# Kernel optimization log

Measured on AMD Instinct MI355X. Metric: run time of the kernel, lower is better.

## Reference

```python
import jax, jax.numpy as jnp
import numpy as np

B, S, D, F, E, K = 4, 2048, 768, 3072, 8, 2
LB_W, Z_W = 0.01, 0.001


def setup_inputs() -> dict:
    key = jax.random.key(0)
    ks = jax.random.split(key, 6)
    x = jax.random.normal(ks[0], (B, S, D), dtype=jnp.float32)
    Wr = jax.random.truncated_normal(ks[1], -2.0, 2.0, (D, E), dtype=jnp.float32) * 0.02
    W1 = jax.random.normal(ks[2], (E, D, F), dtype=jnp.float32) * (1.0 / np.sqrt(D))
    b1 = jnp.zeros((E, F), dtype=jnp.float32)
    W2 = jax.random.normal(ks[3], (E, F, D), dtype=jnp.float32) * (1.0 / np.sqrt(F))
    b2 = jnp.zeros((E, D), dtype=jnp.float32)
    return {"x": x, "Wr": Wr, "W1": W1, "b1": b1, "W2": W2, "b2": b2}


def reference(x, Wr, W1, b1, W2, b2):
    # Router
    router_logits = jnp.einsum('bsd,de->bse', x, Wr)            # [B,S,E]
    router_probs = jax.nn.softmax(router_logits, axis=-1)
    top_k_probs, top_k_idx = jax.lax.top_k(router_probs, K)     # [B,S,K]
    top_k_probs = top_k_probs / (jnp.sum(top_k_probs, axis=-1, keepdims=True) + 1e-8)

    # Auxiliary losses
    expert_usage = jnp.mean(router_probs, axis=(0, 1))          # [E]
    mean_usage = jnp.mean(expert_usage)
    var_usage = jnp.mean(jnp.square(expert_usage - mean_usage))
    lb_loss = var_usage / (mean_usage * mean_usage + 1e-8) * jnp.float32(E)
    z_loss = jnp.mean(jnp.square(jax.nn.logsumexp(router_logits, axis=-1)))

    # Combine weights per expert: sum over top-k slots assigned to expert e
    one_hot = jax.nn.one_hot(top_k_idx, E, dtype=x.dtype)       # [B,S,K,E]
    combine = jnp.sum(one_hot * top_k_probs[..., None], axis=2) # [B,S,E]

    # Expert FFNs (loop over fixed small E, vectorized over tokens)
    output = jnp.zeros_like(x)
    for e in range(E):
        h = jax.nn.gelu(jnp.einsum('bsd,df->bsf', x, W1[e]) + b1[e], approximate=False)
        y = jnp.einsum('bsf,fd->bsd', h, W2[e]) + b2[e]
        output = output + y * combine[..., e:e + 1]

    aux = {"load_balancing_loss": lb_loss * LB_W, "router_z_loss": z_loss * Z_W}
    return output, aux["load_balancing_loss"], aux["router_z_loss"]
```

## Files before the change

### kernel.cpp

```cpp
#include <hip/hip_runtime.h>
#include <cstdint>
#include <cstddef>

#define B_ 4
#define S_ 2048
#define D_ 768
#define F_ 3072
#define E_ 8
#define NTOK (B_*S_)
#define NASSIGN (NTOK*2)
#define RBLK 256
#define FBLK 32
#define MAXTILE 136

typedef unsigned short u16;
typedef __attribute__((ext_vector_type(8))) __bf16 bf16x8;
typedef __attribute__((ext_vector_type(4))) float f32x4;

__device__ __forceinline__ u16 f2bf(float f) {
    unsigned int u = __builtin_bit_cast(unsigned int, f);
    u += 0x7fffu + ((u >> 16) & 1u);
    return (u16)(u >> 16);
}

__device__ __forceinline__ void async16(const void* g, void* l) {
    __builtin_amdgcn_global_load_lds(
        (const __attribute__((address_space(1))) unsigned int*)g,
        (__attribute__((address_space(3))) unsigned int*)l, 16, 0, 0);
}

__device__ __forceinline__ float gelu_f(float v) {
    float z = v * 0.70710678f;
    float a = fabsf(z);
    float t = __builtin_amdgcn_rcpf(1.0f + 0.3275911f * a);
    float poly = t * (0.254829592f + t * (-0.284496736f + t * (1.421413741f +
                 t * (-1.453152027f + t * 1.061405429f))));
    float e = __expf(-z * z);
    float erf_z = copysignf(1.0f - poly * e, z);
    return 0.5f * v * (1.0f + erf_z);
}

__global__ void k_init(int* cursors) {
    int t = threadIdx.x;
    if (t < E_) cursors[t] = 0;
}

__global__ void k_cvt_x(const float* __restrict__ x, u16* __restrict__ xb) {
    int id = blockIdx.x * 256 + threadIdx.x;
    float4 v = ((const float4*)x)[id];
    ushort4 o;
    o.x = f2bf(v.x); o.y = f2bf(v.y); o.z = f2bf(v.z); o.w = f2bf(v.w);
    ((ushort4*)xb)[id] = o;
}

__global__ void k_tcvt(const float* __restrict__ in, u16* __restrict__ out, int R, int C) {
    __shared__ u16 t[32][33];
    int e = blockIdx.z;
    int c0 = blockIdx.x * 32, r0 = blockIdx.y * 32;
    int tx = threadIdx.x & 7;
    int ty = threadIdx.x >> 3;
    const float* ip = in + (size_t)e * R * C + (size_t)(r0 + ty) * C + c0 + tx * 4;
    float4 v = *(const float4*)ip;
    t[tx * 4 + 0][ty] = f2bf(v.x);
    t[tx * 4 + 1][ty] = f2bf(v.y);
    t[tx * 4 + 2][ty] = f2bf(v.z);
    t[tx * 4 + 3][ty] = f2bf(v.w);
    __syncthreads();
    u16* op = out + (size_t)e * C * R + (size_t)(c0 + ty) * R + r0 + tx * 4;
    ushort4 o;
    o.x = t[ty][tx * 4 + 0]; o.y = t[ty][tx * 4 + 1];
    o.z = t[ty][tx * 4 + 2]; o.w = t[ty][tx * 4 + 3];
    *(ushort4*)op = o;
}

__global__ __launch_bounds__(256) void k_router(
    const float* __restrict__ x, const float* __restrict__ Wr,
    float* __restrict__ usage_part,
    float* __restrict__ z_part,
    int*   __restrict__ hist_part,
    int* __restrict__ tk_idx, float* __restrict__ tk_w)
{
    __shared__ float wrt[E_ * D_];
    __shared__ float s_usage[E_];
    __shared__ float s_z;
    __shared__ int   s_hist[E_];
    int tid = threadIdx.x;
    for (int i = tid; i < E_ * D_; i += 256) {
        int d = i >> 3, e = i & 7;
        wrt[e * D_ + d] = Wr[i];
    }
    if (tid < E_) { s_usage[tid] = 0.f; s_hist[tid] = 0; }
    if (tid == 0) s_z = 0.f;
    __syncthreads();

    int w = tid >> 6, lane = tid & 63;
    float u_acc[E_];
    #pragma unroll
    for (int e = 0; e < E_; e++) u_acc[e] = 0.f;
    float z_acc = 0.f;

    for (int it = 0; it < 8; it++) {
        int tok = blockIdx.x * 32 + it * 4 + w;
        float acc[E_];
        #pragma unroll
        for (int e = 0; e < E_; e++) acc[e] = 0.f;
        const float* xr = x + (size_t)tok * D_;
        for (int d = lane; d < D_; d += 64) {
            float xv = xr[d];
            #pragma unroll
            for (int e = 0; e < E_; e++) acc[e] += xv * wrt[e * D_ + d];
        }
        #pragma unroll
        for (int off = 32; off > 0; off >>= 1) {
            #pragma unroll
            for (int e = 0; e < E_; e++) acc[e] += __shfl_down(acc[e], off);
        }
        if (lane == 0) {
            float m = acc[0];
            #pragma unroll
            for (int e = 1; e < E_; e++) m = fmaxf(m, acc[e]);
            float p[E_], s = 0.f;
            #pragma unroll
            for (int e = 0; e < E_; e++) { p[e] = expf(acc[e] - m); s += p[e]; }
            float inv = 1.f / s;
            #pragma unroll
            for (int e = 0; e < E_; e++) { p[e] *= inv; u_acc[e] += p[e]; }
            float lse = m + logf(s);
            z_acc += lse * lse;
            int i1 = 0;
            for (int e = 1; e < E_; e++) if (p[e] > p[i1]) i1 = e;
            int i2 = -1;
            for (int e = 0; e < E_; e++) {
                if (e == i1) continue;
                if (i2 < 0 || p[e] > p[i2]) i2 = e;
            }
            float denom = p[i1] + p[i2] + 1e-8f;
            tk_idx[tok * 2 + 0] = i1; tk_idx[tok * 2 + 1] = i2;
            tk_w[tok * 2 + 0] = p[i1] / denom;
            tk_w[tok * 2 + 1] = p[i2] / denom;
            atomicAdd(&s_hist[i1], 1); atomicAdd(&s_hist[i2], 1);
        }
    }
    if (lane == 0) {
        #pragma unroll
        for (int e = 0; e < E_; e++) atomicAdd(&s_usage[e], u_acc[e]);
        atomicAdd(&s_z, z_acc);
    }
    __syncthreads();
    if (tid < E_) {
        usage_part[blockIdx.x * E_ + tid] = s_usage[tid];
        hist_part[blockIdx.x * E_ + tid]  = s_hist[tid];
    }
    if (tid == 0) z_part[blockIdx.x] = s_z;
}

__global__ __launch_bounds__(256) void k_finalize(
    const float* __restrict__ usage_part, const float* __restrict__ z_part,
    const int* __restrict__ hist_part,
    int* __restrict__ counts, int* __restrict__ offsets,
    int* __restrict__ tile_list,
    float* __restrict__ out_scalars)
{
    __shared__ float s_u[E_];
    __shared__ float s_z;
    __shared__ int   s_h[E_];
    int tid = threadIdx.x;
    if (tid < E_) { s_u[tid] = 0.f; s_h[tid] = 0; }
    if (tid == 0) s_z = 0.f;
    __syncthreads();

    float u[E_]; int h[E_];
    #pragma unroll
    for (int e = 0; e < E_; e++) { u[e] = usage_part[tid * E_ + e]; h[e] = hist_part[tid * E_ + e]; }
    float z = z_part[tid];
    #pragma unroll
    for (int off = 32; off > 0; off >>= 1) {
        #pragma unroll
        for (int e = 0; e < E_; e++) {
            u[e] += __shfl_down(u[e], off);
            h[e] += __shfl_down(h[e], off);
        }
        z += __shfl_down(z, off);
    }
    if ((tid & 63) == 0) {
        #pragma unroll
        for (int e = 0; e < E_; e++) { atomicAdd(&s_u[e], u[e]); atomicAdd(&s_h[e], h[e]); }
        atomicAdd(&s_z, z);
    }
    __syncthreads();
    if (tid == 0) {
        int o = 0, nt = 0;
        for (int e = 0; e < E_; e++) {
            int c = s_h[e];
            counts[e] = c; offsets[e] = o; o += c;
            for (int m0 = 0; m0 < c; m0 += 128) tile_list[1 + nt++] = (m0 << 8) | e;
        }
        tile_list[0] = nt;
        float uu[E_], mean = 0.f;
        for (int e = 0; e < E_; e++) { uu[e] = s_u[e] / (float)NTOK; mean += uu[e]; }
        mean /= (float)E_;
        float var = 0.f;
        for (int e = 0; e < E_; e++) { float d = uu[e] - mean; var += d * d; }
        var /= (float)E_;
        out_scalars[0] = var / (mean * mean + 1e-8f) * (float)E_ * 0.01f;
        out_scalars[1] = (s_z / (float)NTOK) * 0.001f;
    }
}

__global__ __launch_bounds__(256) void k_fill(
    const int* __restrict__ tk_idx, const float* __restrict__ tk_w,
    const int* __restrict__ offsets, int* __restrict__ cursors,
    int* __restrict__ assign_token, float* __restrict__ assign_weight,
    int* __restrict__ pos)
{
    __shared__ int l_cnt[E_];
    __shared__ int l_base[E_];
    int tid = threadIdx.x;
    if (tid < E_) l_cnt[tid] = 0;
    __syncthreads();
    int t = blockIdx.x * 256 + tid;
    int e0 = tk_idx[t * 2 + 0], e1 = tk_idx[t * 2 + 1];
    int r0 = atomicAdd(&l_cnt[e0], 1);
    int r1 = atomicAdd(&l_cnt[e1], 1);
    __syncthreads();
    if (tid < E_) l_base[tid] = atomicAdd(&cursors[tid], l_cnt[tid]);
    __syncthreads();
    int row0 = offsets[e0] + l_base[e0] + r0;
    int row1 = offsets[e1] + l_base[e1] + r1;
    assign_token[row0] = t; assign_weight[row0] = tk_w[t * 2 + 0]; pos[t * 2 + 0] = row0;
    assign_token[row1] = t; assign_weight[row1] = tk_w[t * 2 + 1]; pos[t * 2 + 1] = row1;
}

__global__ __launch_bounds__(256) void k_gemm1(
    const u16* __restrict__ xb, const u16* __restrict__ w1t,
    const float* __restrict__ b1,
    const int* __restrict__ counts, const int* __restrict__ offsets,
    const int* __restrict__ tile_list,
    const int* __restrict__ assign_token, u16* __restrict__ h)
{
    int nt = tile_list[0];
    if ((int)blockIdx.x >= nt) return;
    int packed = tile_list[1 + blockIdx.x];
    int e = packed & 0xff;
    int m0 = packed >> 8;
    int cnt = counts[e];
    int off = offsets[e];
    int n0 = blockIdx.y * 128;

    __shared__ __align__(16) u16 As[2][128 * 32];
    __shared__ __align__(16) u16 Bs[2][128 * 32];

    int tid = threadIdx.x;
    int w = tid >> 6, lane = tid & 63;
    int rA = lane >> 2;
    int colk = (lane & 3) * 8;
    int r0 = (w * 2 + 0) * 16 + rA;
    int r1 = (w * 2 + 1) * 16 + rA;

    int c0b = __builtin_amdgcn_readfirstlane((w * 2 + 0) * 1024);
    int c1b = __builtin_amdgcn_readfirstlane((w * 2 + 1) * 1024);

    int g0 = m0 + r0; if (g0 > cnt - 1) g0 = cnt - 1;
    int g1 = m0 + r1; if (g1 > cnt - 1) g1 = cnt - 1;
    const u16* agp0 = xb + (size_t)assign_token[off + g0] * D_ + colk;
    const u16* agp1 = xb + (size_t)assign_token[off + g1] * D_ + colk;
    const u16* bgp0 = w1t + ((size_t)e * F_ + n0 + r0) * D_ + colk;
    const u16* bgp1 = w1t + ((size_t)e * F_ + n0 + r1) * D_ + colk;

    f32x4 acc[4][4];
    #pragma unroll
    for (int i = 0; i < 4; i++)
        #pragma unroll
        for (int j = 0; j < 4; j++) acc[i][j] = (f32x4){0.f, 0.f, 0.f, 0.f};

    int wm = (w >> 1) * 64, wn = (w & 1) * 64;
    int fm = lane & 15, k8 = (lane >> 4) * 8;

    #define STAGE1(buf, kk) do { \
        async16(agp0 + (kk), (char*)As[buf] + c0b); \
        async16(agp1 + (kk), (char*)As[buf] + c1b); \
        async16(bgp0 + (kk), (char*)Bs[buf] + c0b); \
        async16(bgp1 + (kk), (char*)Bs[buf] + c1b); \
    } while (0)
    #define COMPUTE1(buf) do { \
        bf16x8 af[4], bfr[4]; \
        _Pragma("unroll") \
        for (int i = 0; i < 4; i++) af[i] = *(const bf16x8*)&As[buf][(wm + i * 16 + fm) * 32 + k8]; \
        _Pragma("unroll") \
        for (int j = 0; j < 4; j++) bfr[j] = *(const bf16x8*)&Bs[buf][(wn + j * 16 + fm) * 32 + k8]; \
        _Pragma("unroll") \
        for (int i = 0; i < 4; i++) \
            _Pragma("unroll") \
            for (int j = 0; j < 4; j++) \
                acc[i][j] = __builtin_amdgcn_mfma_f32_16x16x32_bf16(af[i], bfr[j], acc[i][j], 0, 0, 0); \
    } while (0)

    STAGE1(0, 0);
    __syncthreads();
    for (int kk = 0; kk < D_; kk += 64) {
        STAGE1(1, kk + 32);
        COMPUTE1(0);
        __syncthreads();
        if (kk + 64 < D_) STAGE1(0, kk + 64);
        COMPUTE1(1);
        __syncthreads();
    }
    #undef STAGE1
    #undef COMPUTE1

    int rbase = (lane >> 4) * 4;
    #pragma unroll
    for (int j = 0; j < 4; j++) {
        int f = n0 + wn + j * 16 + fm;
        float bias = b1[e * F_ + f];
        #pragma unroll
        for (int i = 0; i < 4; i++) {
            #pragma unroll
            for (int r = 0; r < 4; r++) {
                int m = m0 + wm + i * 16 + rbase + r;
                if (m < cnt) {
                    float v = acc[i][j][r] + bias;
                    h[(size_t)(off + m) * F_ + f] = f2bf(gelu_f(v));
                }
            }
        }
    }
}

__global__ __launch_bounds__(256) void k_gemm2(
    const u16* __restrict__ h, const u16* __restrict__ w2t,
    const float* __restrict__ b2,
    const int* __restrict__ counts, const int* __restrict__ offsets,
    const int* __restrict__ tile_list,
    const float* __restrict__ assign_weight, float* __restrict__ y)
{
    int nt = tile_list[0];
    if ((int)blockIdx.x >= nt) return;
    int packed = tile_list[1 + blockIdx.x];
    int e = packed & 0xff;
    int m0 = packed >> 8;
    int cnt = counts[e];
    int off = offsets[e];
    int n0 = blockIdx.y * 128;

    __shared__ __align__(16) u16 As[2][128 * 32];
    __shared__ __align__(16) u16 Bs[2][128 * 32];

    int tid = threadIdx.x;
    int w = tid >> 6, lane = tid & 63;
    int rA = lane >> 2;
    int colk = (lane & 3) * 8;
    int r0 = (w * 2 + 0) * 16 + rA;
    int r1 = (w * 2 + 1) * 16 + rA;

    int c0b = __builtin_amdgcn_readfirstlane((w * 2 + 0) * 1024);
    int c1b = __builtin_amdgcn_readfirstlane((w * 2 + 1) * 1024);

    const u16* agp0 = h + (size_t)(off + m0 + r0) * F_ + colk;
    const u16* agp1 = h + (size_t)(off + m0 + r1) * F_ + colk;
    const u16* bgp0 = w2t + ((size_t)e * D_ + n0 + r0) * F_ + colk;
    const u16* bgp1 = w2t + ((size_t)e * D_ + n0 + r1) * F_ + colk;

    f32x4 acc[4][4];
    #pragma unroll
    for (int i = 0; i < 4; i++)
        #pragma unroll
        for (int j = 0; j < 4; j++) acc[i][j] = (f32x4){0.f, 0.f, 0.f, 0.f};

    int wm = (w >> 1) * 64, wn = (w & 1) * 64;
    int fm = lane & 15, k8 = (lane >> 4) * 8;

    #define STAGE2(buf, kk) do { \
        async16(agp0 + (kk), (char*)As[buf] + c0b); \
        async16(agp1 + (kk), (char*)As[buf] + c1b); \
        async16(bgp0 + (kk), (char*)Bs[buf] + c0b); \
        async16(bgp1 + (kk), (char*)Bs[buf] + c1b); \
    } while (0)
    #define COMPUTE2(buf) do { \
        bf16x8 af[4], bfr[4]; \
        _Pragma("unroll") \
        for (int i = 0; i < 4; i++) af[i] = *(const bf16x8*)&As[buf][(wm + i * 16 + fm) * 32 + k8]; \
        _Pragma("unroll") \
        for (int j = 0; j < 4; j++) bfr[j] = *(const bf16x8*)&Bs[buf][(wn + j * 16 + fm) * 32 + k8]; \
        _Pragma("unroll") \
        for (int i = 0; i < 4; i++) \
            _Pragma("unroll") \
            for (int j = 0; j < 4; j++) \
                acc[i][j] = __builtin_amdgcn_mfma_f32_16x16x32_bf16(af[i], bfr[j], acc[i][j], 0, 0, 0); \
    } while (0)

    STAGE2(0, 0);
    __syncthreads();
    for (int kk = 0; kk < F_; kk += 64) {
        STAGE2(1, kk + 32);
        COMPUTE2(0);
        __syncthreads();
        if (kk + 64 < F_) STAGE2(0, kk + 64);
        COMPUTE2(1);
        __syncthreads();
    }
    #undef STAGE2
    #undef COMPUTE2

    int rbase = (lane >> 4) * 4;
    #pragma unroll
    for (int j = 0; j < 4; j++) {
        int d = n0 + wn + j * 16 + fm;
        float bias = b2[e * D_ + d];
        #pragma unroll
        for (int i = 0; i < 4; i++) {
            #pragma unroll
            for (int r = 0; r < 4; r++) {
                int m = m0 + wm + i * 16 + rbase + r;
                if (m < cnt) {
                    float wgt = assign_weight[off + m];
                    y[(size_t)(off + m) * D_ + d] = (acc[i][j][r] + bias) * wgt;
                }
            }
        }
    }
}

__global__ void k_combine(const float* __restrict__ y, const int* __restrict__ pos,
                          float* __restrict__ out)
{
    int g = blockIdx.x * 256 + threadIdx.x;
    int t = g / 192, c = g - t * 192;
    int p0 = pos[t * 2], p1 = pos[t * 2 + 1];
    const float4* y4 = (const float4*)y;
    float4 a = y4[(size_t)p0 * 192 + c];
    float4 b = y4[(size_t)p1 * 192 + c];
    float4 o = {a.x + b.x, a.y + b.y, a.z + b.z, a.w + b.w};
    ((float4*)out)[g] = o;
}

extern "C" void kernel_launch(void* const* d_in, const int* in_sizes, int n_in,
                              void* d_out, int out_size, void* d_ws, size_t ws_size,
                              hipStream_t stream)
{
    const float* x  = (const float*)d_in[0];
    const float* Wr = (const float*)d_in[1];
    const float* W1 = (const float*)d_in[2];
    const float* b1 = (const float*)d_in[3];
    const float* W2 = (const float*)d_in[4];
    const float* b2 = (const float*)d_in[5];
    float* out = (float*)d_out;

    char* base = (char*)d_ws;
    size_t o = 0;
    auto alloc = [&](size_t bytes) {
        char* r = base + o;
        o += (bytes + 255) & ~(size_t)255;
        return r;
    };
    int*   counts        = (int*)  alloc(E_ * 4);
    int*   cursors       = (int*)  alloc(E_ * 4);
    int*   offsets       = (int*)  alloc(E_ * 4);
    int*   tile_list     = (int*)  alloc(256 * 4);
    float* usage_part    = (float*)alloc((size_t)RBLK * E_ * 4);
    float* z_part        = (float*)alloc((size_t)RBLK * 4);
    int*   hist_part     = (int*)  alloc((size_t)RBLK * E_ * 4);
    int*   tk_idx        = (int*)  alloc((size_t)NTOK * 2 * 4);
    float* tk_w          = (float*)alloc((size_t)NTOK * 2 * 4);
    int*   pos           = (int*)  alloc((size_t)NTOK * 2 * 4);
    int*   assign_token  = (int*)  alloc((size_t)NASSIGN * 4);
    float* assign_weight = (float*)alloc((size_t)NASSIGN * 4);
    u16*   xb            = (u16*)  alloc((size_t)NTOK * D_ * 2);
    u16*   w1t           = (u16*)  alloc((size_t)E_ * F_ * D_ * 2);
    u16*   w2t           = (u16*)  alloc((size_t)E_ * D_ * F_ * 2);
    u16*   hbuf          = (u16*)  alloc((size_t)NASSIGN * F_ * 2);
    float* y             = (float*)alloc((size_t)NASSIGN * D_ * 4);

    k_init<<<dim3(1), dim3(64), 0, stream>>>(cursors);
    k_cvt_x<<<dim3(NTOK * D_ / 1024), dim3(256), 0, stream>>>(x, xb);
    k_tcvt<<<dim3(F_ / 32, D_ / 32, E_), dim3(256), 0, stream>>>(W1, w1t, D_, F_);
    k_tcvt<<<dim3(D_ / 32, F_ / 32, E_), dim3(256), 0, stream>>>(W2, w2t, F_, D_);
    k_router<<<dim3(RBLK), dim3(256), 0, stream>>>(x, Wr, usage_part, z_part, hist_part, tk_idx, tk_w);
    k_finalize<<<dim3(1), dim3(256), 0, stream>>>(usage_part, z_part, hist_part, counts, offsets,
                                                  tile_list, out + (size_t)NTOK * D_);
    k_fill<<<dim3(FBLK), dim3(256), 0, stream>>>(tk_idx, tk_w, offsets, cursors, assign_token, assign_weight, pos);
    k_gemm1<<<dim3(MAXTILE, F_ / 128), dim3(256), 0, stream>>>(xb, w1t, b1, counts, offsets, tile_list,
                                                               assign_token, hbuf);
    k_gemm2<<<dim3(MAXTILE, D_ / 128), dim3(256), 0, stream>>>(hbuf, w2t, b2, counts, offsets, tile_list,
                                                               assign_weight, y);
    k_combine<<<dim3(NTOK * D_ / 1024), dim3(256), 0, stream>>>(y, pos, out);
}
```

Before: 624.0 us.

## Swizzle LDS tiles, stage gemm1 epilogue via LDS, fuse combine into gemm2 atomics

Applies an XOR swizzle to the LDS tile layout in both grouped GEMMs to cut bank conflicts on the MFMA fragment reads. The gemm1 epilogue is staged through LDS so GELU outputs go to global memory as 16-byte row stores instead of scattered 2-byte writes. The gemm2 epilogue scatters weighted results straight into the output with float atomic adds after a memset, which removes the y buffer, the pos array and the combine kernel. The atomics add contention and make the float summation order nondeterministic, and hbuf is padded to cover the tail tile's writes.

Result: faster. 611.6 us (-2.0%).

```diff
diff --git a/kernel.cpp b/kernel.cpp
--- a/kernel.cpp
+++ b/kernel.cpp
@@ -75,9 +75,8 @@
 
 __global__ __launch_bounds__(256) void k_router(
     const float* __restrict__ x, const float* __restrict__ Wr,
-    float* __restrict__ usage_part,
-    float* __restrict__ z_part,
-    int*   __restrict__ hist_part,
+    float* __restrict__ usage_part, float* __restrict__ z_part,
+    int* __restrict__ hist_part,
     int* __restrict__ tk_idx, float* __restrict__ tk_w)
 {
     __shared__ float wrt[E_ * D_];
@@ -210,8 +209,7 @@
 __global__ __launch_bounds__(256) void k_fill(
     const int* __restrict__ tk_idx, const float* __restrict__ tk_w,
     const int* __restrict__ offsets, int* __restrict__ cursors,
-    int* __restrict__ assign_token, float* __restrict__ assign_weight,
-    int* __restrict__ pos)
+    int* __restrict__ assign_token, float* __restrict__ assign_weight)
 {
     __shared__ int l_cnt[E_];
     __shared__ int l_base[E_];
@@ -227,8 +225,8 @@
     __syncthreads();
     int row0 = offsets[e0] + l_base[e0] + r0;
     int row1 = offsets[e1] + l_base[e1] + r1;
-    assign_token[row0] = t; assign_weight[row0] = tk_w[t * 2 + 0]; pos[t * 2 + 0] = row0;
-    assign_token[row1] = t; assign_weight[row1] = tk_w[t * 2 + 1]; pos[t * 2 + 1] = row1;
+    assign_token[row0] = t; assign_weight[row0] = tk_w[t * 2 + 0];
+    assign_token[row1] = t; assign_weight[row1] = tk_w[t * 2 + 1];
 }
 
 __global__ __launch_bounds__(256) void k_gemm1(
@@ -247,13 +245,13 @@
     int off = offsets[e];
     int n0 = blockIdx.y * 128;
 
-    __shared__ __align__(16) u16 As[2][128 * 32];
-    __shared__ __align__(16) u16 Bs[2][128 * 32];
+    __shared__ __align__(16) u16 SM[16384];
+    char* smb = (char*)SM;
 
     int tid = threadIdx.x;
     int w = tid >> 6, lane = tid & 63;
     int rA = lane >> 2;
-    int colk = (lane & 3) * 8;
+    int colk = ((lane & 3) ^ (rA & 3)) * 8;
     int r0 = (w * 2 + 0) * 16 + rA;
     int r1 = (w * 2 + 1) * 16 + rA;
 
@@ -274,20 +272,23 @@
         for (int j = 0; j < 4; j++) acc[i][j] = (f32x4){0.f, 0.f, 0.f, 0.f};
 
     int wm = (w >> 1) * 64, wn = (w & 1) * 64;
-    int fm = lane & 15, k8 = (lane >> 4) * 8;
+    int fm = lane & 15;
+    int slot = ((lane >> 4) ^ (fm & 3)) * 8;
 
     #define STAGE1(buf, kk) do { \
-        async16(agp0 + (kk), (char*)As[buf] + c0b); \
-        async16(agp1 + (kk), (char*)As[buf] + c1b); \
-        async16(bgp0 + (kk), (char*)Bs[buf] + c0b); \
-        async16(bgp1 + (kk), (char*)Bs[buf] + c1b); \
+        async16(agp0 + (kk), smb + (buf) * 8192 + c0b); \
+        async16(agp1 + (kk), smb + (buf) * 8192 + c1b); \
+        async16(bgp0 + (kk), smb + 16384 + (buf) * 8192 + c0b); \
+        async16(bgp1 + (kk), smb + 16384 + (buf) * 8192 + c1b); \
     } while (0)
     #define COMPUTE1(buf) do { \
+        const u16* Ab = SM + (buf) * 4096; \
+        const u16* Bb = SM + 8192 + (buf) * 4096; \
         bf16x8 af[4], bfr[4]; \
         _Pragma("unroll") \
-        for (int i = 0; i < 4; i++) af[i] = *(const bf16x8*)&As[buf][(wm + i * 16 + fm) * 32 + k8]; \
-        _Pragma("unroll") \
-        for (int j = 0; j < 4; j++) bfr[j] = *(const bf16x8*)&Bs[buf][(wn + j * 16 + fm) * 32 + k8]; \
+        for (int i = 0; i < 4; i++) af[i] = *(const bf16x8*)&Ab[(wm + i * 16 + fm) * 32 + slot]; \
+        _Pragma("unroll") \
+        for (int j = 0; j < 4; j++) bfr[j] = *(const bf16x8*)&Bb[(wn + j * 16 + fm) * 32 + slot]; \
         _Pragma("unroll") \
         for (int i = 0; i < 4; i++) \
             _Pragma("unroll") \
@@ -309,21 +310,30 @@
     #undef COMPUTE1
 
     int rbase = (lane >> 4) * 4;
-    #pragma unroll
-    for (int j = 0; j < 4; j++) {
-        int f = n0 + wn + j * 16 + fm;
-        float bias = b1[e * F_ + f];
-        #pragma unroll
-        for (int i = 0; i < 4; i++) {
+    u16* tb = SM + w * 4096;
+    float biasv[4];
+    #pragma unroll
+    for (int j = 0; j < 4; j++) biasv[j] = b1[e * F_ + n0 + wn + j * 16 + fm];
+    #pragma unroll
+    for (int i = 0; i < 4; i++)
+        #pragma unroll
+        for (int j = 0; j < 4; j++)
             #pragma unroll
             for (int r = 0; r < 4; r++) {
-                int m = m0 + wm + i * 16 + rbase + r;
-                if (m < cnt) {
-                    float v = acc[i][j][r] + bias;
-                    h[(size_t)(off + m) * F_ + f] = f2bf(gelu_f(v));
-                }
+                int m_l = i * 16 + rbase + r;
+                int f_l = j * 16 + fm;
+                u16 q = f2bf(gelu_f(acc[i][j][r] + biasv[j]));
+                tb[m_l * 64 + ((((f_l >> 3) ^ (m_l & 7)) << 3) | (f_l & 7))] = q;
             }
-        }
+    __syncthreads();
+    #pragma unroll
+    for (int s = 0; s < 8; s++) {
+        int m_l = s * 8 + (lane >> 3);
+        int c = lane & 7;
+        uint4 vv = *(const uint4*)&tb[m_l * 64 + ((c ^ (m_l & 7)) << 3)];
+        int m = m0 + wm + m_l;
+        if (m < cnt)
+            *(uint4*)&h[(size_t)(off + m) * F_ + n0 + wn + c * 8] = vv;
     }
 }
 
@@ -332,7 +342,8 @@
     const float* __restrict__ b2,
     const int* __restrict__ counts, const int* __restrict__ offsets,
     const int* __restrict__ tile_list,
-    const float* __restrict__ assign_weight, float* __restrict__ y)
+    const int* __restrict__ assign_token, const float* __restrict__ assign_weight,
+    float* __restrict__ out)
 {
     int nt = tile_list[0];
     if ((int)blockIdx.x >= nt) return;
@@ -343,13 +354,13 @@
     int off = offsets[e];
     int n0 = blockIdx.y * 128;
 
-    __shared__ __align__(16) u16 As[2][128 * 32];
-    __shared__ __align__(16) u16 Bs[2][128 * 32];
+    __shared__ __align__(16) u16 SM[16384];
+    char* smb = (char*)SM;
 
     int tid = threadIdx.x;
     int w = tid >> 6, lane = tid & 63;
     int rA = lane >> 2;
-    int colk = (lane & 3) * 8;
+    int colk = ((lane & 3) ^ (rA & 3)) * 8;
     int r0 = (w * 2 + 0) * 16 + rA;
     int r1 = (w * 2 + 1) * 16 + rA;
 
@@ -368,20 +379,23 @@
         for (int j = 0; j < 4; j++) acc[i][j] = (f32x4){0.f, 0.f, 0.f, 0.f};
 
     int wm = (w >> 1) * 64, wn = (w & 1) * 64;
-    int fm = lane & 15, k8 = (lane >> 4) * 8;
+    int fm = lane & 15;
+    int slot = ((lane >> 4) ^ (fm & 3)) * 8;
 
     #define STAGE2(buf, kk) do { \
-        async16(agp0 + (kk), (char*)As[buf] + c0b); \
-        async16(agp1 + (kk), (char*)As[buf] + c1b); \
-        async16(bgp0 + (kk), (char*)Bs[buf] + c0b); \
-        async16(bgp1 + (kk), (char*)Bs[buf] + c1b); \
+        async16(agp0 + (kk), smb + (buf) * 8192 + c0b); \
+        async16(agp1 + (kk), smb + (buf) * 8192 + c1b); \
+        async16(bgp0 + (kk), smb + 16384 + (buf) * 8192 + c0b); \
+        async16(bgp1 + (kk), smb + 16384 + (buf) * 8192 + c1b); \
     } while (0)
     #define COMPUTE2(buf) do { \
+        const u16* Ab = SM + (buf) * 4096; \
+        const u16* Bb = SM + 8192 + (buf) * 4096; \
         bf16x8 af[4], bfr[4]; \
         _Pragma("unroll") \
-        for (int i = 0; i < 4; i++) af[i] = *(const bf16x8*)&As[buf][(wm + i * 16 + fm) * 32 + k8]; \
-        _Pragma("unroll") \
-        for (int j = 0; j < 4; j++) bfr[j] = *(const bf16x8*)&Bs[buf][(wn + j * 16 + fm) * 32 + k8]; \
+        for (int i = 0; i < 4; i++) af[i] = *(const bf16x8*)&Ab[(wm + i * 16 + fm) * 32 + slot]; \
+        _Pragma("unroll") \
+        for (int j = 0; j < 4; j++) bfr[j] = *(const bf16x8*)&Bb[(wn + j * 16 + fm) * 32 + slot]; \
         _Pragma("unroll") \
         for (int i = 0; i < 4; i++) \
             _Pragma("unroll") \
@@ -403,35 +417,23 @@
     #undef COMPUTE2
 
     int rbase = (lane >> 4) * 4;
-    #pragma unroll
-    for (int j = 0; j < 4; j++) {
-        int d = n0 + wn + j * 16 + fm;
-        float bias = b2[e * D_ + d];
-        #pragma unroll
-        for (int i = 0; i < 4; i++) {
-            #pragma unroll
-            for (int r = 0; r < 4; r++) {
-                int m = m0 + wm + i * 16 + rbase + r;
-                if (m < cnt) {
-                    float wgt = assign_weight[off + m];
-                    y[(size_t)(off + m) * D_ + d] = (acc[i][j][r] + bias) * wgt;
-                }
+    float biasv[4];
+    #pragma unroll
+    for (int j = 0; j < 4; j++) biasv[j] = b2[e * D_ + n0 + wn + j * 16 + fm];
+    #pragma unroll
+    for (int i = 0; i < 4; i++)
+        #pragma unroll
+        for (int r = 0; r < 4; r++) {
+            int m = m0 + wm + i * 16 + rbase + r;
+            if (m < cnt) {
+                int t = assign_token[off + m];
+                float wg = assign_weight[off + m];
+                float* orow = out + (size_t)t * D_ + n0 + wn + fm;
+                #pragma unroll
+                for (int j = 0; j < 4; j++)
+                    unsafeAtomicAdd(orow + j * 16, (acc[i][j][r] + biasv[j]) * wg);
             }
         }
-    }
-}
-
-__global__ void k_combine(const float* __restrict__ y, const int* __restrict__ pos,
-                          float* __restrict__ out)
-{
-    int g = blockIdx.x * 256 + threadIdx.x;
-    int t = g / 192, c = g - t * 192;
-    int p0 = pos[t * 2], p1 = pos[t * 2 + 1];
-    const float4* y4 = (const float4*)y;
-    float4 a = y4[(size_t)p0 * 192 + c];
-    float4 b = y4[(size_t)p1 * 192 + c];
-    float4 o = {a.x + b.x, a.y + b.y, a.z + b.z, a.w + b.w};
-    ((float4*)out)[g] = o;
 }
 
 extern "C" void kernel_launch(void* const* d_in, const int* in_sizes, int n_in,
@@ -462,15 +464,14 @@
     int*   hist_part     = (int*)  alloc((size_t)RBLK * E_ * 4);
     int*   tk_idx        = (int*)  alloc((size_t)NTOK * 2 * 4);
     float* tk_w          = (float*)alloc((size_t)NTOK * 2 * 4);
-    int*   pos           = (int*)  alloc((size_t)NTOK * 2 * 4);
     int*   assign_token  = (int*)  alloc((size_t)NASSIGN * 4);
     float* assign_weight = (float*)alloc((size_t)NASSIGN * 4);
     u16*   xb            = (u16*)  alloc((size_t)NTOK * D_ * 2);
     u16*   w1t           = (u16*)  alloc((size_t)E_ * F_ * D_ * 2);
     u16*   w2t           = (u16*)  alloc((size_t)E_ * D_ * F_ * 2);
-    u16*   hbuf          = (u16*)  alloc((size_t)NASSIGN * F_ * 2);
-    float* y             = (float*)alloc((size_t)NASSIGN * D_ * 4);
-
+    u16*   hbuf          = (u16*)  alloc((size_t)(NASSIGN + 128) * F_ * 2);
+
+    hipMemsetAsync(d_out, 0, (size_t)out_size * 4, stream);
     k_init<<<dim3(1), dim3(64), 0, stream>>>(cursors);
     k_cvt_x<<<dim3(NTOK * D_ / 1024), dim3(256), 0, stream>>>(x, xb);
     k_tcvt<<<dim3(F_ / 32, D_ / 32, E_), dim3(256), 0, stream>>>(W1, w1t, D_, F_);
@@ -478,10 +479,9 @@
     k_router<<<dim3(RBLK), dim3(256), 0, stream>>>(x, Wr, usage_part, z_part, hist_part, tk_idx, tk_w);
     k_finalize<<<dim3(1), dim3(256), 0, stream>>>(usage_part, z_part, hist_part, counts, offsets,
                                                   tile_list, out + (size_t)NTOK * D_);
-    k_fill<<<dim3(FBLK), dim3(256), 0, stream>>>(tk_idx, tk_w, offsets, cursors, assign_token, assign_weight, pos);
+    k_fill<<<dim3(FBLK), dim3(256), 0, stream>>>(tk_idx, tk_w, offsets, cursors, assign_token, assign_weight);
     k_gemm1<<<dim3(MAXTILE, F_ / 128), dim3(256), 0, stream>>>(xb, w1t, b1, counts, offsets, tile_list,
                                                                assign_token, hbuf);
     k_gemm2<<<dim3(MAXTILE, D_ / 128), dim3(256), 0, stream>>>(hbuf, w2t, b2, counts, offsets, tile_list,
-                                                               assign_weight, y);
-    k_combine<<<dim3(NTOK * D_ / 1024), dim3(256), 0, stream>>>(y, pos, out);
-}
+                                                               assign_token, assign_weight, out);
+}
```
